# Optimization experiments

Measured on AMD Instinct MI355X. Metric: run time of the kernel, lower is better.

The kernel has to match this reference:

```python
import jax, jax.numpy as jnp
import numpy as np

B, T, E, H = 4, 1024, 1024, 16
D = E // H  # head_size = 64
EPS = 1e-5


def layernorm(x, g, b):
    mu = jnp.mean(x, axis=-1, keepdims=True)
    var = jnp.mean(jnp.square(x - mu), axis=-1, keepdims=True)
    return (x - mu) * jax.lax.rsqrt(var + EPS) * g + b


def setup_inputs() -> dict:
    key = jax.random.key(0)
    ks = jax.random.split(key, 12)
    s = 0.02
    return {
        "x": jax.random.normal(ks[0], (B, T, E), dtype=jnp.float32),
        "ln1_g": jnp.ones((E,), jnp.float32),
        "ln1_b": jnp.zeros((E,), jnp.float32),
        "Wq": jax.random.normal(ks[1], (H, E, D), dtype=jnp.float32) * s,
        "Wk": jax.random.normal(ks[2], (H, E, D), dtype=jnp.float32) * s,
        "Wv": jax.random.normal(ks[3], (H, E, D), dtype=jnp.float32) * s,
        "Wp": jax.random.normal(ks[4], (E, E), dtype=jnp.float32) * s,
        "bp": jnp.zeros((E,), jnp.float32),
        "ln2_g": jnp.ones((E,), jnp.float32),
        "ln2_b": jnp.zeros((E,), jnp.float32),
        "W1": jax.random.normal(ks[5], (E, 4 * E), dtype=jnp.float32) * s,
        "b1": jnp.zeros((4 * E,), jnp.float32),
        "W2": jax.random.normal(ks[6], (4 * E, E), dtype=jnp.float32) * s,
        "b2": jnp.zeros((E,), jnp.float32),
    }


def reference(x, ln1_g, ln1_b, Wq, Wk, Wv, Wp, bp, ln2_g, ln2_b, W1, b1, W2, b2):
    # --- attention sub-block (pre-LN) ---
    h = layernorm(x, ln1_g, ln1_b)               # [B,T,E]
    q = jnp.einsum('bte,hed->bhtd', h, Wq)       # [B,H,T,D]
    k = jnp.einsum('bte,hed->bhtd', h, Wk)
    v = jnp.einsum('bte,hed->bhtd', h, Wv)
    # NOTE: original module has NO 1/sqrt(D) scaling and its 'tril' buffer is
    # all-ones, so masked_fill is a no-op -> full (non-causal) softmax.
    scores = jnp.einsum('bhtd,bhsd->bhts', q, k)  # [B,H,T,T]
    attn = jax.nn.softmax(scores, axis=-1)
    o = jnp.einsum('bhts,bhsd->bhtd', attn, v)    # [B,H,T,D]
    o = o.transpose(0, 2, 1, 3).reshape(x.shape[0], x.shape[1], -1)  # [B,T,E]
    x = x + o @ Wp + bp
    # --- feedforward sub-block (dropout is identity at eval) ---
    h2 = layernorm(x, ln2_g, ln2_b)
    x = x + jax.nn.relu(h2 @ W1 + b1) @ W2 + b2
    return x
```

## Files before the change

### kernel.cpp

```cpp
#include <hip/hip_runtime.h>
#include <hip/hip_bf16.h>

#define BB 4
#define TT 1024
#define EE 1024
#define HH 16
#define DD 64
#define MM 4096
#define NQKV 3072
#define E4 4096

using short8  = __attribute__((ext_vector_type(8))) short;
using short4v = __attribute__((ext_vector_type(4))) short;
using f32x4   = __attribute__((ext_vector_type(4))) float;

__device__ __forceinline__ short f2bf(float f) {
    __hip_bfloat16 h = __float2bfloat16(f);
    return *reinterpret_cast<short*>(&h);
}

__device__ __forceinline__ unsigned int cvtpk_bf16(float a, float b) {
    unsigned int w;
    asm("v_cvt_pk_bf16_f32 %0, %1, %2" : "=v"(w) : "v"(a), "v"(b));
    return w;
}

__device__ __forceinline__ void gld16(const void* g, void* l) {
    __builtin_amdgcn_global_load_lds((__attribute__((address_space(1))) void*)g,
                                     (__attribute__((address_space(3))) void*)l,
                                     16, 0, 0);
}

__global__ __launch_bounds__(256) void tcvt_kernel(const float* __restrict__ in,
                                                   short* __restrict__ out,
                                                   int R, int C) {
    __shared__ short tile[64][65];
    const int c0 = blockIdx.x * 64, r0 = blockIdx.y * 64;
    const int tr = threadIdx.x >> 6;
    const int tc = threadIdx.x & 63;
#pragma unroll
    for (int i = 0; i < 16; ++i) {
        int r = i * 4 + tr;
        tile[tc][r] = f2bf(in[(size_t)(r0 + r) * C + c0 + tc]);
    }
    __syncthreads();
#pragma unroll
    for (int i = 0; i < 16; ++i) {
        int c = i * 4 + tr;
        out[(size_t)(c0 + c) * R + r0 + tc] = tile[c][tc];
    }
}

__global__ __launch_bounds__(256) void pack_qkv_t(const float* __restrict__ Wq,
                                                  const float* __restrict__ Wk,
                                                  const float* __restrict__ Wv,
                                                  short* __restrict__ out) {
    __shared__ short tile[64][65];
    const int m = blockIdx.y;
    const int which = m >> 4, head = m & 15;
    const float* src = ((which == 0) ? Wq : (which == 1) ? Wk : Wv) + (size_t)head * EE * DD;
    const float scale = (which == 1) ? 1.44269504f : 1.0f;
    const int e0 = blockIdx.x * 64;
    const int tr = threadIdx.x >> 6, tc = threadIdx.x & 63;
#pragma unroll
    for (int i = 0; i < 16; ++i) {
        int e = i * 4 + tr;
        tile[tc][e] = f2bf(src[(size_t)(e0 + e) * DD + tc] * scale);
    }
    __syncthreads();
#pragma unroll
    for (int i = 0; i < 16; ++i) {
        int d = i * 4 + tr;
        out[(size_t)(which * 1024 + head * 64 + d) * EE + e0 + tc] = tile[d][tc];
    }
}

__global__ __launch_bounds__(256) void vtr_kernel(const short* __restrict__ qkv,
                                                  short* __restrict__ vT) {
    __shared__ short tile[64][68];
    const int b = blockIdx.z;
    const int t0 = blockIdx.x * 64, c0 = blockIdx.y * 64;
    const int tr = threadIdx.x >> 4;
    const int q4 = (threadIdx.x & 15) * 4;
#pragma unroll
    for (int i = 0; i < 4; ++i) {
        int t = i * 16 + tr;
        short4v v = *(const short4v*)&qkv[((size_t)b * TT + t0 + t) * NQKV + 2048 + c0 + q4];
        *(short4v*)&tile[t][q4] = v;
    }
    __syncthreads();
#pragma unroll
    for (int i = 0; i < 4; ++i) {
        int c = i * 16 + tr;
        short4v v;
        v[0] = tile[q4 + 0][c];
        v[1] = tile[q4 + 1][c];
        v[2] = tile[q4 + 2][c];
        v[3] = tile[q4 + 3][c];
        *(short4v*)&vT[((size_t)b * 1024 + c0 + c) * TT + t0 + q4] = v;
    }
}

__global__ __launch_bounds__(256) void ln_kernel(const float* __restrict__ x,
                                                 const float* __restrict__ g,
                                                 const float* __restrict__ b,
                                                 short* __restrict__ out) {
    __shared__ float red[4];
    const int row = blockIdx.x;
    const int tid = threadIdx.x;
    float4 v = *(const float4*)&x[(size_t)row * EE + tid * 4];
    float s = v.x + v.y + v.z + v.w;
#pragma unroll
    for (int off = 32; off >= 1; off >>= 1) s += __shfl_xor(s, off, 64);
    if ((tid & 63) == 0) red[tid >> 6] = s;
    __syncthreads();
    float mean = (red[0] + red[1] + red[2] + red[3]) * (1.0f / EE);
    __syncthreads();
    float d0 = v.x - mean, d1 = v.y - mean, d2 = v.z - mean, d3 = v.w - mean;
    s = d0 * d0 + d1 * d1 + d2 * d2 + d3 * d3;
#pragma unroll
    for (int off = 32; off >= 1; off >>= 1) s += __shfl_xor(s, off, 64);
    if ((tid & 63) == 0) red[tid >> 6] = s;
    __syncthreads();
    float var = (red[0] + red[1] + red[2] + red[3]) * (1.0f / EE);
    float rstd = rsqrtf(var + 1e-5f);
    int c = tid * 4;
    short4v o;
    o[0] = f2bf(d0 * rstd * g[c + 0] + b[c + 0]);
    o[1] = f2bf(d1 * rstd * g[c + 1] + b[c + 1]);
    o[2] = f2bf(d2 * rstd * g[c + 2] + b[c + 2]);
    o[3] = f2bf(d3 * rstd * g[c + 3] + b[c + 3]);
    *(short4v*)&out[(size_t)row * EE + c] = o;
}

__global__ __launch_bounds__(256) void redk4_kernel(const float* __restrict__ p012,
                                                    const float* __restrict__ p3,
                                                    const float* __restrict__ bias,
                                                    const float* __restrict__ resid,
                                                    float* __restrict__ out) {
    const size_t i = ((size_t)blockIdx.x * 256 + threadIdx.x) * 4;
    float4 a = *(const float4*)&p012[i];
    float4 b = *(const float4*)&p012[i + (size_t)MM * EE];
    float4 c = *(const float4*)&p012[i + (size_t)2 * MM * EE];
    float4 d = *(const float4*)&p3[i];
    float4 r = *(const float4*)&resid[i];
    float4 bb = *(const float4*)&bias[i & 1023];
    float4 o;
    o.x = (a.x + b.x) + (c.x + d.x) + r.x + bb.x;
    o.y = (a.y + b.y) + (c.y + d.y) + r.y + bb.y;
    o.z = (a.z + b.z) + (c.z + d.z) + r.z + bb.z;
    o.w = (a.w + b.w) + (c.w + d.w) + r.w + bb.w;
    *(float4*)&out[i] = o;
}

template <bool HAS_BIAS, bool RELU, bool SPLIT>
__global__ __launch_bounds__(512, 2) void gemm256(const short* __restrict__ A,
                                                  const short* __restrict__ Bt,
                                                  const float* __restrict__ bias,
                                                  void* __restrict__ outp,
                                                  void* __restrict__ outp3,
                                                  int M, int N, int K, int lda) {
    __shared__ __align__(16) short Ab[2][2][8192];
    __shared__ __align__(16) short Bb[2][2][8192];

    const int tid = threadIdx.x;
    const int lane = tid & 63;
    const int wid = tid >> 6;
    const int wr = wid >> 2;
    const int wc = wid & 3;
    const int l15 = lane & 15, lhi = lane >> 4;
    const int rsw = l15 & 7;

    int wg = blockIdx.y * gridDim.x + blockIdx.x;
    const int chunk = (gridDim.x * gridDim.y) >> 3;
    wg = (wg & 7) * chunk + (wg >> 3);
    const int bx = wg % gridDim.x, by = wg / gridDim.x;
    const int row0 = by * 256, col0 = bx * 256;

    const int kb = SPLIT ? blockIdx.z * K : 0;

    const int srow = tid >> 3;
    const int scol = (((tid & 7) ^ (srow & 7)) << 3);

    const int NT = K >> 6;

    f32x4 acc[8][4] = {};

    auto stageA = [&](int b, int h, int k0) {
#pragma unroll
        for (int j = 0; j < 2; ++j)
            gld16(&A[(size_t)(row0 + h * 128 + j * 64 + srow) * lda + kb + k0 + scol],
                  &Ab[b][h][j * 4096 + wid * 512]);
    };
    auto stageB = [&](int b, int h, int k0) {
#pragma unroll
        for (int j = 0; j < 2; ++j)
            gld16(&Bt[(size_t)(col0 + h * 128 + j * 64 + srow) * lda + kb + k0 + scol],
                  &Bb[b][h][j * 4096 + wid * 512]);
    };

    stageA(0, 0, 0); stageA(0, 1, 0);
    stageB(0, 0, 0); stageB(0, 1, 0);
    if (NT > 1) {
        stageB(1, 0, 64); stageB(1, 1, 64);
        asm volatile("s_waitcnt vmcnt(4)" ::: "memory");
    } else {
        asm volatile("s_waitcnt vmcnt(0)" ::: "memory");
    }
    __builtin_amdgcn_s_barrier();

    for (int u = 0; u < NT; ++u) {
        const int buf = u & 1;
        short8 bfr[4][2];
#pragma unroll
        for (int p = 0; p < 4; ++p) {
            if (p == 0) {
#pragma unroll
                for (int n = 0; n < 4; ++n)
#pragma unroll
                    for (int ks = 0; ks < 2; ++ks)
                        bfr[n][ks] = *(const short8*)&Bb[buf][wc >> 1]
                            [((wc & 1) * 64 + n * 16 + l15) * 64 +
                             (((ks << 2) + lhi) ^ rsw) * 8];
            }
            short8 af[2][2];
#pragma unroll
            for (int mi = 0; mi < 2; ++mi)
#pragma unroll
                for (int ks = 0; ks < 2; ++ks)
                    af[mi][ks] = *(const short8*)&Ab[buf][wr]
                        [((p * 2 + mi) * 16 + l15) * 64 +
                         (((ks << 2) + lhi) ^ rsw) * 8];
            if (p == 0 && u + 1 < NT) stageA(buf ^ 1, 0, (u + 1) << 6);
            if (p == 1 && u + 1 < NT) stageA(buf ^ 1, 1, (u + 1) << 6);
            if (p == 2 && u + 2 < NT) stageB(buf, 0, (u + 2) << 6);
            if (p == 3 && u + 2 < NT) stageB(buf, 1, (u + 2) << 6);
            __builtin_amdgcn_s_barrier();
            __builtin_amdgcn_s_setprio(1);
#pragma unroll
            for (int mi = 0; mi < 2; ++mi)
#pragma unroll
                for (int n = 0; n < 4; ++n)
#pragma unroll
                    for (int ks = 0; ks < 2; ++ks)
                        acc[p * 2 + mi][n] = __builtin_amdgcn_mfma_f32_16x16x32_bf16(
                            af[mi][ks], bfr[n][ks], acc[p * 2 + mi][n], 0, 0, 0);
            __builtin_amdgcn_s_setprio(0);
            if (p == 3 && u + 1 < NT) {
                if (u + 2 < NT) asm volatile("s_waitcnt vmcnt(4)" ::: "memory");
                else            asm volatile("s_waitcnt vmcnt(0)" ::: "memory");
            }
            __builtin_amdgcn_s_barrier();
        }
    }

    short* outb = (short*)outp;
    float* outf = nullptr;
    if (SPLIT)
        outf = (blockIdx.z == 3) ? (float*)outp3
                                 : (float*)outp + (size_t)blockIdx.z * M * N;
#pragma unroll
    for (int m = 0; m < 8; ++m)
#pragma unroll
        for (int n = 0; n < 4; ++n)
#pragma unroll
            for (int r = 0; r < 4; ++r) {
                int row = row0 + wr * 128 + m * 16 + lhi * 4 + r;
                int col = col0 + wc * 64 + n * 16 + l15;
                float v = acc[m][n][r];
                if (SPLIT) {
                    outf[(size_t)row * N + col] = v;
                } else {
                    if (HAS_BIAS) v += bias[col];
                    if (RELU) v = fmaxf(v, 0.f);
                    outb[(size_t)row * N + col] = f2bf(v);
                }
            }
}

template <int BN, int PIPE, bool HAS_BIAS, bool RELU, bool RESID, bool OUT_BF16>
__global__ __launch_bounds__(256) void gemm_bt(const short* __restrict__ A,
                                               const short* __restrict__ Bt,
                                               const float* __restrict__ bias,
                                               const float* __restrict__ resid,
                                               void* __restrict__ outp,
                                               int M, int N, int K) {
    constexpr int WRC = (BN == 128) ? 2 : 4;
    constexpr int WCC = (BN == 128) ? 2 : 1;
    constexpr int MI = 8 / WRC;
    constexpr int NI = BN / (16 * WCC);
    constexpr int BCH = BN / 32;
    constexpr int ASZ = 128 * 64, BSZ = BN * 64;

    __shared__ __align__(16) short As[(PIPE ? 2 : 1) * ASZ];
    __shared__ __align__(16) short Bs[(PIPE ? 2 : 1) * BSZ];

    const int tid = threadIdx.x;
    const int lane = tid & 63;
    const int wid = tid >> 6;
    const int wr = (WRC == 2) ? (wid >> 1) : wid;
    const int wc = (WCC == 2) ? (wid & 1) : 0;
    const int l15 = lane & 15, lhi = lane >> 4;

    int wg = blockIdx.y * gridDim.x + blockIdx.x;
    const int chunk = (gridDim.x * gridDim.y) >> 3;
    wg = (wg & 7) * chunk + (wg >> 3);
    const int bx = wg % gridDim.x;
    const int by = wg / gridDim.x;
    const int row0 = by * 128, col0 = bx * BN;

    const int srow = tid >> 3;
    const int scol = (((tid & 7) ^ (srow & 7)) << 3);
    const int rsw = l15 & 7;

    const int wrow0 = wr * (16 * MI);
    const int wcol0 = wc * (16 * NI);

    f32x4 acc[MI][NI] = {};

    auto stage = [&](int k0, int bs) {
#pragma unroll
        for (int ch = 0; ch < 4; ++ch)
            gld16(&A[(size_t)(row0 + ch * 32 + srow) * K + k0 + scol],
                  &As[bs * ASZ + ch * 2048 + wid * 512]);
#pragma unroll
        for (int ch = 0; ch < BCH; ++ch)
            gld16(&Bt[(size_t)(col0 + ch * 32 + srow) * K + k0 + scol],
                  &Bs[bs * BSZ + ch * 2048 + wid * 512]);
    };
    auto compute = [&](int bs) {
#pragma unroll
        for (int ks = 0; ks < 2; ++ks) {
            short8 af[MI], bf[NI];
#pragma unroll
            for (int mi = 0; mi < MI; ++mi)
                af[mi] = *(const short8*)&As[bs * ASZ + (wrow0 + mi * 16 + l15) * 64 +
                                             (((ks << 2) + lhi) ^ rsw) * 8];
#pragma unroll
            for (int ni = 0; ni < NI; ++ni)
                bf[ni] = *(const short8*)&Bs[bs * BSZ + (wcol0 + ni * 16 + l15) * 64 +
                                             (((ks << 2) + lhi) ^ rsw) * 8];
#pragma unroll
            for (int mi = 0; mi < MI; ++mi)
#pragma unroll
                for (int ni = 0; ni < NI; ++ni)
                    acc[mi][ni] = __builtin_amdgcn_mfma_f32_16x16x32_bf16(
                        af[mi], bf[ni], acc[mi][ni], 0, 0, 0);
        }
    };

    if (PIPE == 1) {
        const int nt = K >> 6;
        stage(0, 0);
        stage(64, 1);
        int cur = 0;
        for (int t = 0; t < nt; ++t) {
            if (t + 1 < nt) asm volatile("s_waitcnt vmcnt(6)" ::: "memory");
            else            asm volatile("s_waitcnt vmcnt(0)" ::: "memory");
            __builtin_amdgcn_s_barrier();
            __builtin_amdgcn_sched_barrier(0);
            compute(cur);
            __builtin_amdgcn_sched_barrier(0);
            __builtin_amdgcn_s_barrier();
            if (t + 2 < nt) stage((t + 2) << 6, cur);
            cur ^= 1;
        }
    } else {
        for (int k0 = 0; k0 < K; k0 += 64) {
            __syncthreads();
            stage(k0, 0);
            __syncthreads();
            compute(0);
        }
    }

    float* outf = (float*)outp;
    short* outb = (short*)outp;
#pragma unroll
    for (int mi = 0; mi < MI; ++mi)
#pragma unroll
        for (int ni = 0; ni < NI; ++ni)
#pragma unroll
            for (int r = 0; r < 4; ++r) {
                int row = row0 + wrow0 + mi * 16 + lhi * 4 + r;
                int col = col0 + wcol0 + ni * 16 + l15;
                float v = acc[mi][ni][r];
                if (HAS_BIAS) v += bias[col];
                if (RELU) v = fmaxf(v, 0.f);
                if (RESID) v += resid[(size_t)row * N + col];
                if (OUT_BF16) outb[(size_t)row * N + col] = f2bf(v);
                else outf[(size_t)row * N + col] = v;
            }
}

__global__ __launch_bounds__(256) void attn_kernel(const short* __restrict__ qkv,
                                                   const short* __restrict__ vT,
                                                   short* __restrict__ obuf) {
    __shared__ __align__(16) short Ks[2][64 * 64];
    __shared__ __align__(16) short Vs[2][64 * 64];
    __shared__ __align__(16) unsigned int Pl[4][2][16][40];
    const int tid = threadIdx.x;
    const int lane = tid & 63;
    const int wid = tid >> 6;
    const int l15 = lane & 15, lhi = lane >> 4;
    const int lhi4 = lhi * 4;

    const int nb = ((blockIdx.x & 7) << 6) + (blockIdx.x >> 3);
    const int b = nb >> 7;
    const int h = (nb >> 3) & 15;
    const int q0 = (nb & 7) << 7;
    const size_t rbase = (size_t)b * TT;
    const int hq = h * 64;
    const short* vg = vT + ((size_t)b * 1024 + hq) * TT;

    const int srow = tid >> 3;
    const int scol = (((tid & 7) ^ (srow & 7)) << 3);
    const int rsw = (l15 & 7);

    short8 aq[2][2];
#pragma unroll
    for (int g = 0; g < 2; ++g)
#pragma unroll
        for (int ks = 0; ks < 2; ++ks)
            aq[g][ks] = *(const short8*)&qkv[(rbase + q0 + wid * 32 + g * 16 + l15) * NQKV +
                                             hq + ks * 32 + lhi * 8];

    float mrun[2] = {-INFINITY, -INFINITY};
    float lsum[2] = {0.f, 0.f};
    f32x4 o[2][4] = {};

#pragma unroll
    for (int ch = 0; ch < 2; ++ch) {
        gld16(&qkv[(rbase + 0 + ch * 32 + srow) * NQKV + 1024 + hq + scol],
              &Ks[0][ch * 2048 + wid * 512]);
        gld16(&vg[(size_t)(ch * 32 + srow) * TT + 0 + scol],
              &Vs[0][ch * 2048 + wid * 512]);
    }
    __syncthreads();

    int cur = 0;
    for (int st = 0; st < TT; st += 64) {
        if (st + 64 < TT) {
#pragma unroll
            for (int ch = 0; ch < 2; ++ch) {
                gld16(&qkv[(rbase + st + 64 + ch * 32 + srow) * NQKV + 1024 + hq + scol],
                      &Ks[cur ^ 1][ch * 2048 + wid * 512]);
                gld16(&vg[(size_t)(ch * 32 + srow) * TT + st + 64 + scol],
                      &Vs[cur ^ 1][ch * 2048 + wid * 512]);
            }
        }
        const short* K = &Ks[cur][0];
        const short* V = &Vs[cur][0];

        short8 kf[4][2];
#pragma unroll
        for (int nt = 0; nt < 4; ++nt)
#pragma unroll
            for (int ks = 0; ks < 2; ++ks)
                kf[nt][ks] = *(const short8*)&K[(nt * 16 + l15) * 64 +
                                               (((ks << 2) + lhi) ^ rsw) * 8];

        short8 pa[2][2];
#pragma unroll
        for (int g = 0; g < 2; ++g) {
            f32x4 stv[4] = {};
            __builtin_amdgcn_s_setprio(1);
#pragma unroll
            for (int nt = 0; nt < 4; ++nt)
#pragma unroll
                for (int ks = 0; ks < 2; ++ks)
                    stv[nt] = __builtin_amdgcn_mfma_f32_16x16x32_bf16(
                        kf[nt][ks], aq[g][ks], stv[nt], 0, 0, 0);
            __builtin_amdgcn_s_setprio(0);
            float tn[4];
#pragma unroll
            for (int nt = 0; nt < 4; ++nt)
                tn[nt] = fmaxf(fmaxf(stv[nt][0], stv[nt][1]),
                               fmaxf(stv[nt][2], stv[nt][3]));
            float tm = fmaxf(fmaxf(tn[0], tn[1]), fmaxf(tn[2], tn[3]));
            tm = fmaxf(tm, __shfl_xor(tm, 16, 64));
            tm = fmaxf(tm, __shfl_xor(tm, 32, 64));
            const bool full = !__all(tm - mrun[g] <= 11.5f);
            if (full) {
                float mnew = fmaxf(mrun[g], tm);
                float fac = exp2f(mrun[g] - mnew);
                mrun[g] = mnew;
                lsum[g] *= fac;
                float f0 = __shfl(fac, lhi4 + 0, 64);
                float f1 = __shfl(fac, lhi4 + 1, 64);
                float f2 = __shfl(fac, lhi4 + 2, 64);
                float f3 = __shfl(fac, lhi4 + 3, 64);
#pragma unroll
                for (int dt = 0; dt < 4; ++dt) {
                    o[g][dt][0] *= f0; o[g][dt][1] *= f1;
                    o[g][dt][2] *= f2; o[g][dt][3] *= f3;
                }
            }
            float pv[4][4];
            float sn[4];
#pragma unroll
            for (int nt = 0; nt < 4; ++nt) {
#pragma unroll
                for (int r = 0; r < 4; ++r) pv[nt][r] = exp2f(stv[nt][r] - mrun[g]);
                sn[nt] = (pv[nt][0] + pv[nt][1]) + (pv[nt][2] + pv[nt][3]);
            }
            float rs = (sn[0] + sn[1]) + (sn[2] + sn[3]);
            rs += __shfl_xor(rs, 16, 64);
            rs += __shfl_xor(rs, 32, 64);
            lsum[g] += rs;
#pragma unroll
            for (int nt = 0; nt < 4; ++nt) {
                uint2 ww;
                ww.x = cvtpk_bf16(pv[nt][0], pv[nt][1]);
                ww.y = cvtpk_bf16(pv[nt][2], pv[nt][3]);
                *(uint2*)&Pl[wid][g][l15][nt * 8 + lhi * 2] = ww;
            }
            pa[g][0] = *(const short8*)&Pl[wid][g][l15][lhi4];
            pa[g][1] = *(const short8*)&Pl[wid][g][l15][16 + lhi4];
        }

        short8 vf[4][2];
#pragma unroll
        for (int dt = 0; dt < 4; ++dt)
#pragma unroll
            for (int k2 = 0; k2 < 2; ++k2)
                vf[dt][k2] = *(const short8*)&V[(dt * 16 + l15) * 64 +
                                               (((k2 << 2) + lhi) ^ rsw) * 8];
        __builtin_amdgcn_s_setprio(1);
#pragma unroll
        for (int g = 0; g < 2; ++g)
#pragma unroll
            for (int dt = 0; dt < 4; ++dt)
#pragma unroll
                for (int k2 = 0; k2 < 2; ++k2)
                    o[g][dt] = __builtin_amdgcn_mfma_f32_16x16x32_bf16(
                        pa[g][k2], vf[dt][k2], o[g][dt], 0, 0, 0);
        __builtin_amdgcn_s_setprio(0);

        __syncthreads();
        cur ^= 1;
    }
#pragma unroll
    for (int g = 0; g < 2; ++g) {
        float inv = 1.0f / lsum[g];
        float i0 = __shfl(inv, lhi4 + 0, 64);
        float i1 = __shfl(inv, lhi4 + 1, 64);
        float i2 = __shfl(inv, lhi4 + 2, 64);
        float i3 = __shfl(inv, lhi4 + 3, 64);
#pragma unroll
        for (int dt = 0; dt < 4; ++dt) {
            int col = hq + dt * 16 + l15;
            size_t rw = rbase + q0 + wid * 32 + g * 16 + lhi4;
            obuf[(rw + 0) * EE + col] = f2bf(o[g][dt][0] * i0);
            obuf[(rw + 1) * EE + col] = f2bf(o[g][dt][1] * i1);
            obuf[(rw + 2) * EE + col] = f2bf(o[g][dt][2] * i2);
            obuf[(rw + 3) * EE + col] = f2bf(o[g][dt][3] * i3);
        }
    }
}

extern "C" void kernel_launch(void* const* d_in, const int* in_sizes, int n_in,
                              void* d_out, int out_size, void* d_ws, size_t ws_size,
                              hipStream_t stream) {
    const float* x   = (const float*)d_in[0];
    const float* g1  = (const float*)d_in[1];
    const float* be1 = (const float*)d_in[2];
    const float* Wq  = (const float*)d_in[3];
    const float* Wk  = (const float*)d_in[4];
    const float* Wv  = (const float*)d_in[5];
    const float* Wp  = (const float*)d_in[6];
    const float* bp  = (const float*)d_in[7];
    const float* g2  = (const float*)d_in[8];
    const float* be2 = (const float*)d_in[9];
    const float* W1  = (const float*)d_in[10];
    const float* b1f = (const float*)d_in[11];
    const float* W2  = (const float*)d_in[12];
    const float* b2f = (const float*)d_in[13];

    char* p = (char*)d_ws;
    short* h_bf   = (short*)p; p += (size_t)MM * EE * 2;
    short* wqkv   = (short*)p; p += (size_t)EE * NQKV * 2;
    short* qkv    = (short*)p; p += (size_t)MM * NQKV * 2;
    short* o_bf   = (short*)p; p += (size_t)MM * EE * 2;
    short* wp_bf  = (short*)p; p += (size_t)EE * EE * 2;
    float* x1     = (float*)p; p += (size_t)MM * EE * 4;
    short* h2_bf  = (short*)p; p += (size_t)MM * EE * 2;
    short* w1_bf  = (short*)p; p += (size_t)EE * E4 * 2;
    short* mid_bf = (short*)p; p += (size_t)MM * E4 * 2;
    short* w2_bf  = (short*)p; p += (size_t)E4 * EE * 2;
    short* vTb    = (short*)p; p += (size_t)BB * 1024 * TT * 2;

    float* part012 = (float*)d_ws;
    float* part3   = (float*)h2_bf;

    pack_qkv_t<<<dim3(16, 48), 256, 0, stream>>>(Wq, Wk, Wv, wqkv);
    tcvt_kernel<<<dim3(16, 16), 256, 0, stream>>>(Wp, wp_bf, EE, EE);
    tcvt_kernel<<<dim3(64, 16), 256, 0, stream>>>(W1, w1_bf, EE, E4);
    tcvt_kernel<<<dim3(16, 64), 256, 0, stream>>>(W2, w2_bf, E4, EE);

    ln_kernel<<<MM, 256, 0, stream>>>(x, g1, be1, h_bf);

    gemm256<false, false, false>
        <<<dim3(NQKV / 256, MM / 256), 512, 0, stream>>>(h_bf, wqkv, nullptr,
                                                         qkv, nullptr, MM, NQKV, EE, EE);

    vtr_kernel<<<dim3(16, 16, BB), 256, 0, stream>>>(qkv, vTb);

    attn_kernel<<<BB * HH * (TT / 128), 256, 0, stream>>>(qkv, vTb, o_bf);

    gemm_bt<64, 1, true, false, true, false>
        <<<dim3(EE / 64, MM / 128), 256, 0, stream>>>(o_bf, wp_bf, bp, x, x1, MM, EE, EE);

    ln_kernel<<<MM, 256, 0, stream>>>(x1, g2, be2, h2_bf);

    gemm256<true, true, false>
        <<<dim3(E4 / 256, MM / 256), 512, 0, stream>>>(h2_bf, w1_bf, b1f,
                                                       mid_bf, nullptr, MM, E4, EE, EE);

    gemm256<false, false, true>
        <<<dim3(EE / 256, MM / 256, 4), 512, 0, stream>>>(mid_bf, w2_bf, nullptr,
                                                          part012, part3,
                                                          MM, EE, 1024, E4);
    redk4_kernel<<<(MM * EE / 4) / 256, 256, 0, stream>>>(part012, part3, b2f, x1,
                                                          (float*)d_out);
}
```

Baseline: 225.5 us.

## Enlarge attention blocks to 256 queries and 128-key tiles with 8 waves

The attention kernel now runs 512 threads per block covering 256 query rows, and stages 128 keys per iteration instead of 64. Each staged K/V tile is reused by twice as many waves, and the kernel does half as many barrier and double-buffer iterations. The V tile uses a new 128-wide swizzled layout, and the P scratch buffer shrinks to one slot per wave. The cost is more LDS per block and half as many blocks (256), which may reduce occupancy and load balance across CUs.

```diff
diff --git a/kernel.cpp b/kernel.cpp
--- a/kernel.cpp
+++ b/kernel.cpp
@@ -393,29 +393,31 @@
             }
 }
 
-__global__ __launch_bounds__(256) void attn_kernel(const short* __restrict__ qkv,
+__global__ __launch_bounds__(512) void attn_kernel(const short* __restrict__ qkv,
                                                    const short* __restrict__ vT,
                                                    short* __restrict__ obuf) {
-    __shared__ __align__(16) short Ks[2][64 * 64];
-    __shared__ __align__(16) short Vs[2][64 * 64];
-    __shared__ __align__(16) unsigned int Pl[4][2][16][40];
+    __shared__ __align__(16) short Ks[2][128 * 64];
+    __shared__ __align__(16) short Vs[2][64 * 128];
+    __shared__ __align__(16) unsigned int Pl[8][16][40];
     const int tid = threadIdx.x;
     const int lane = tid & 63;
     const int wid = tid >> 6;
     const int l15 = lane & 15, lhi = lane >> 4;
     const int lhi4 = lhi * 4;
 
-    const int nb = ((blockIdx.x & 7) << 6) + (blockIdx.x >> 3);
-    const int b = nb >> 7;
-    const int h = (nb >> 3) & 15;
-    const int q0 = (nb & 7) << 7;
+    const int nb = ((blockIdx.x & 7) << 5) + (blockIdx.x >> 3);
+    const int b = nb >> 6;
+    const int h = (nb >> 2) & 15;
+    const int q0 = (nb & 3) << 8;
     const size_t rbase = (size_t)b * TT;
     const int hq = h * 64;
     const short* vg = vT + ((size_t)b * 1024 + hq) * TT;
 
     const int srow = tid >> 3;
     const int scol = (((tid & 7) ^ (srow & 7)) << 3);
-    const int rsw = (l15 & 7);
+    const int vrow = tid >> 4;
+    const int vscol = ((tid & 15) ^ (vrow & 7)) << 3;
+    const int rsw = l15 & 7;
 
     short8 aq[2][2];
 #pragma unroll
@@ -429,113 +431,112 @@
     float lsum[2] = {0.f, 0.f};
     f32x4 o[2][4] = {};
 
-#pragma unroll
-    for (int ch = 0; ch < 2; ++ch) {
-        gld16(&qkv[(rbase + 0 + ch * 32 + srow) * NQKV + 1024 + hq + scol],
-              &Ks[0][ch * 2048 + wid * 512]);
-        gld16(&vg[(size_t)(ch * 32 + srow) * TT + 0 + scol],
-              &Vs[0][ch * 2048 + wid * 512]);
-    }
+    auto stage = [&](int buf, int st) {
+#pragma unroll
+        for (int ch = 0; ch < 2; ++ch)
+            gld16(&qkv[(rbase + st + ch * 64 + srow) * NQKV + 1024 + hq + scol],
+                  &Ks[buf][ch * 4096 + wid * 512]);
+#pragma unroll
+        for (int ch = 0; ch < 2; ++ch)
+            gld16(&vg[(size_t)(ch * 32 + vrow) * TT + st + vscol],
+                  &Vs[buf][ch * 4096 + wid * 512]);
+    };
+
+    stage(0, 0);
     __syncthreads();
 
     int cur = 0;
-    for (int st = 0; st < TT; st += 64) {
-        if (st + 64 < TT) {
-#pragma unroll
-            for (int ch = 0; ch < 2; ++ch) {
-                gld16(&qkv[(rbase + st + 64 + ch * 32 + srow) * NQKV + 1024 + hq + scol],
-                      &Ks[cur ^ 1][ch * 2048 + wid * 512]);
-                gld16(&vg[(size_t)(ch * 32 + srow) * TT + st + 64 + scol],
-                      &Vs[cur ^ 1][ch * 2048 + wid * 512]);
-            }
-        }
+    for (int st = 0; st < TT; st += 128) {
+        if (st + 128 < TT) stage(cur ^ 1, st + 128);
         const short* K = &Ks[cur][0];
         const short* V = &Vs[cur][0];
 
-        short8 kf[4][2];
-#pragma unroll
-        for (int nt = 0; nt < 4; ++nt)
-#pragma unroll
-            for (int ks = 0; ks < 2; ++ks)
-                kf[nt][ks] = *(const short8*)&K[(nt * 16 + l15) * 64 +
-                                               (((ks << 2) + lhi) ^ rsw) * 8];
-
-        short8 pa[2][2];
-#pragma unroll
-        for (int g = 0; g < 2; ++g) {
-            f32x4 stv[4] = {};
+#pragma unroll
+        for (int h2 = 0; h2 < 2; ++h2) {
+            short8 kf[4][2];
+#pragma unroll
+            for (int nt = 0; nt < 4; ++nt)
+#pragma unroll
+                for (int ks = 0; ks < 2; ++ks)
+                    kf[nt][ks] = *(const short8*)&K[(h2 * 64 + nt * 16 + l15) * 64 +
+                                                   (((ks << 2) + lhi) ^ rsw) * 8];
+
+            short8 pa[2][2];
+#pragma unroll
+            for (int g = 0; g < 2; ++g) {
+                f32x4 stv[4] = {};
+                __builtin_amdgcn_s_setprio(1);
+#pragma unroll
+                for (int nt = 0; nt < 4; ++nt)
+#pragma unroll
+                    for (int ks = 0; ks < 2; ++ks)
+                        stv[nt] = __builtin_amdgcn_mfma_f32_16x16x32_bf16(
+                            kf[nt][ks], aq[g][ks], stv[nt], 0, 0, 0);
+                __builtin_amdgcn_s_setprio(0);
+                float tn[4];
+#pragma unroll
+                for (int nt = 0; nt < 4; ++nt)
+                    tn[nt] = fmaxf(fmaxf(stv[nt][0], stv[nt][1]),
+                                   fmaxf(stv[nt][2], stv[nt][3]));
+                float tm = fmaxf(fmaxf(tn[0], tn[1]), fmaxf(tn[2], tn[3]));
+                tm = fmaxf(tm, __shfl_xor(tm, 16, 64));
+                tm = fmaxf(tm, __shfl_xor(tm, 32, 64));
+                const bool full = !__all(tm - mrun[g] <= 11.5f);
+                if (full) {
+                    float mnew = fmaxf(mrun[g], tm);
+                    float fac = exp2f(mrun[g] - mnew);
+                    mrun[g] = mnew;
+                    lsum[g] *= fac;
+                    float f0 = __shfl(fac, lhi4 + 0, 64);
+                    float f1 = __shfl(fac, lhi4 + 1, 64);
+                    float f2 = __shfl(fac, lhi4 + 2, 64);
+                    float f3 = __shfl(fac, lhi4 + 3, 64);
+#pragma unroll
+                    for (int dt = 0; dt < 4; ++dt) {
+                        o[g][dt][0] *= f0; o[g][dt][1] *= f1;
+                        o[g][dt][2] *= f2; o[g][dt][3] *= f3;
+                    }
+                }
+                float pv[4][4], sn[4];
+#pragma unroll
+                for (int nt = 0; nt < 4; ++nt) {
+#pragma unroll
+                    for (int r = 0; r < 4; ++r) pv[nt][r] = exp2f(stv[nt][r] - mrun[g]);
+                    sn[nt] = (pv[nt][0] + pv[nt][1]) + (pv[nt][2] + pv[nt][3]);
+                }
+                float rs = (sn[0] + sn[1]) + (sn[2] + sn[3]);
+                rs += __shfl_xor(rs, 16, 64);
+                rs += __shfl_xor(rs, 32, 64);
+                lsum[g] += rs;
+#pragma unroll
+                for (int nt = 0; nt < 4; ++nt) {
+                    uint2 ww;
+                    ww.x = cvtpk_bf16(pv[nt][0], pv[nt][1]);
+                    ww.y = cvtpk_bf16(pv[nt][2], pv[nt][3]);
+                    *(uint2*)&Pl[wid][l15][nt * 8 + lhi * 2] = ww;
+                }
+                pa[g][0] = *(const short8*)&Pl[wid][l15][lhi4];
+                pa[g][1] = *(const short8*)&Pl[wid][l15][16 + lhi4];
+            }
+
+            short8 vf[4][2];
+#pragma unroll
+            for (int dt = 0; dt < 4; ++dt)
+#pragma unroll
+                for (int k2 = 0; k2 < 2; ++k2)
+                    vf[dt][k2] = *(const short8*)&V[(dt * 16 + l15) * 128 +
+                                                   ((h2 << 3) + (((k2 << 2) + lhi) ^ rsw)) * 8];
             __builtin_amdgcn_s_setprio(1);
 #pragma unroll
-            for (int nt = 0; nt < 4; ++nt)
-#pragma unroll
-                for (int ks = 0; ks < 2; ++ks)
-                    stv[nt] = __builtin_amdgcn_mfma_f32_16x16x32_bf16(
-                        kf[nt][ks], aq[g][ks], stv[nt], 0, 0, 0);
+            for (int g = 0; g < 2; ++g)
+#pragma unroll
+                for (int dt = 0; dt < 4; ++dt)
+#pragma unroll
+                    for (int k2 = 0; k2 < 2; ++k2)
+                        o[g][dt] = __builtin_amdgcn_mfma_f32_16x16x32_bf16(
+                            pa[g][k2], vf[dt][k2], o[g][dt], 0, 0, 0);
             __builtin_amdgcn_s_setprio(0);
-            float tn[4];
-#pragma unroll
-            for (int nt = 0; nt < 4; ++nt)
-                tn[nt] = fmaxf(fmaxf(stv[nt][0], stv[nt][1]),
-                               fmaxf(stv[nt][2], stv[nt][3]));
-            float tm = fmaxf(fmaxf(tn[0], tn[1]), fmaxf(tn[2], tn[3]));
-            tm = fmaxf(tm, __shfl_xor(tm, 16, 64));
-            tm = fmaxf(tm, __shfl_xor(tm, 32, 64));
-            const bool full = !__all(tm - mrun[g] <= 11.5f);
-            if (full) {
-                float mnew = fmaxf(mrun[g], tm);
-                float fac = exp2f(mrun[g] - mnew);
-                mrun[g] = mnew;
-                lsum[g] *= fac;
-                float f0 = __shfl(fac, lhi4 + 0, 64);
-                float f1 = __shfl(fac, lhi4 + 1, 64);
-                float f2 = __shfl(fac, lhi4 + 2, 64);
-                float f3 = __shfl(fac, lhi4 + 3, 64);
-#pragma unroll
-                for (int dt = 0; dt < 4; ++dt) {
-                    o[g][dt][0] *= f0; o[g][dt][1] *= f1;
-                    o[g][dt][2] *= f2; o[g][dt][3] *= f3;
-                }
-            }
-            float pv[4][4];
-            float sn[4];
-#pragma unroll
-            for (int nt = 0; nt < 4; ++nt) {
-#pragma unroll
-                for (int r = 0; r < 4; ++r) pv[nt][r] = exp2f(stv[nt][r] - mrun[g]);
-                sn[nt] = (pv[nt][0] + pv[nt][1]) + (pv[nt][2] + pv[nt][3]);
-            }
-            float rs = (sn[0] + sn[1]) + (sn[2] + sn[3]);
-            rs += __shfl_xor(rs, 16, 64);
-            rs += __shfl_xor(rs, 32, 64);
-            lsum[g] += rs;
-#pragma unroll
-            for (int nt = 0; nt < 4; ++nt) {
-                uint2 ww;
-                ww.x = cvtpk_bf16(pv[nt][0], pv[nt][1]);
-                ww.y = cvtpk_bf16(pv[nt][2], pv[nt][3]);
-                *(uint2*)&Pl[wid][g][l15][nt * 8 + lhi * 2] = ww;
-            }
-            pa[g][0] = *(const short8*)&Pl[wid][g][l15][lhi4];
-            pa[g][1] = *(const short8*)&Pl[wid][g][l15][16 + lhi4];
         }
-
-        short8 vf[4][2];
-#pragma unroll
-        for (int dt = 0; dt < 4; ++dt)
-#pragma unroll
-            for (int k2 = 0; k2 < 2; ++k2)
-                vf[dt][k2] = *(const short8*)&V[(dt * 16 + l15) * 64 +
-                                               (((k2 << 2) + lhi) ^ rsw) * 8];
-        __builtin_amdgcn_s_setprio(1);
-#pragma unroll
-        for (int g = 0; g < 2; ++g)
-#pragma unroll
-            for (int dt = 0; dt < 4; ++dt)
-#pragma unroll
-                for (int k2 = 0; k2 < 2; ++k2)
-                    o[g][dt] = __builtin_amdgcn_mfma_f32_16x16x32_bf16(
-                        pa[g][k2], vf[dt][k2], o[g][dt], 0, 0, 0);
-        __builtin_amdgcn_s_setprio(0);
 
         __syncthreads();
         cur ^= 1;
@@ -606,7 +607,7 @@
 
     vtr_kernel<<<dim3(16, 16, BB), 256, 0, stream>>>(qkv, vTb);
 
-    attn_kernel<<<BB * HH * (TT / 128), 256, 0, stream>>>(qkv, vTb, o_bf);
+    attn_kernel<<<BB * HH * (TT / 256), 512, 0, stream>>>(qkv, vTb, o_bf);
 
     gemm_bt<64, 1, true, false, true, false>
         <<<dim3(EE / 64, MM / 128), 256, 0, stream>>>(o_bf, wp_bf, bp, x, x1, MM, EE, EE);
```

Result: no change. 221.9 us (-1.6%).

## Split attention over two KV halves with separate combine kernel

Applied to the files above, without the earlier changes.

Doubles the attention grid by giving each block half of the key/value sequence, writing unnormalized fp32 partial outputs plus running max and sum. A new combine kernel merges the two halves with log-sum-exp weights and writes the bf16 head-interleaved output. This aims to raise occupancy and parallelism on a grid that was small relative to the CU count, at the cost of extra fp32 partial traffic and an additional launch. Partials reuse existing workspace buffers.

```diff
diff --git a/kernel.cpp b/kernel.cpp
--- a/kernel.cpp
+++ b/kernel.cpp
@@ -151,6 +151,27 @@
     o.z = (a.z + b.z) + (c.z + d.z) + r.z + bb.z;
     o.w = (a.w + b.w) + (c.w + d.w) + r.w + bb.w;
     *(float4*)&out[i] = o;
+}
+
+__global__ __launch_bounds__(256) void comb_kernel(const float* __restrict__ pO,
+                                                   const float2* __restrict__ pml,
+                                                   short* __restrict__ obuf) {
+    const int row = blockIdx.x * 16 + (threadIdx.x >> 4);
+    const int d = (threadIdx.x & 15) * 4;
+    float2 ml0 = pml[row];
+    float2 ml1 = pml[row + 65536];
+    float m = fmaxf(ml0.x, ml1.x);
+    float w0 = exp2f(ml0.x - m), w1 = exp2f(ml1.x - m);
+    float inv = 1.0f / (w0 * ml0.y + w1 * ml1.y);
+    float4 O0 = *(const float4*)&pO[(size_t)row * 64 + d];
+    float4 O1 = *(const float4*)&pO[(size_t)(row + 65536) * 64 + d];
+    short4v s;
+    s[0] = f2bf((O0.x * w0 + O1.x * w1) * inv);
+    s[1] = f2bf((O0.y * w0 + O1.y * w1) * inv);
+    s[2] = f2bf((O0.z * w0 + O1.z * w1) * inv);
+    s[3] = f2bf((O0.w * w0 + O1.w * w1) * inv);
+    const int b = row >> 14, h = (row >> 10) & 15, q = row & 1023;
+    *(short4v*)&obuf[((size_t)b * 1024 + q) * EE + h * 64 + d] = s;
 }
 
 template <bool HAS_BIAS, bool RELU, bool SPLIT>
@@ -395,20 +416,23 @@
 
 __global__ __launch_bounds__(256) void attn_kernel(const short* __restrict__ qkv,
                                                    const short* __restrict__ vT,
-                                                   short* __restrict__ obuf) {
+                                                   float* __restrict__ pO,
+                                                   float2* __restrict__ pml) {
     __shared__ __align__(16) short Ks[2][64 * 64];
     __shared__ __align__(16) short Vs[2][64 * 64];
-    __shared__ __align__(16) unsigned int Pl[4][2][16][40];
+    __shared__ __align__(16) unsigned int Pl[4][16][44];
     const int tid = threadIdx.x;
     const int lane = tid & 63;
     const int wid = tid >> 6;
     const int l15 = lane & 15, lhi = lane >> 4;
     const int lhi4 = lhi * 4;
 
-    const int nb = ((blockIdx.x & 7) << 6) + (blockIdx.x >> 3);
-    const int b = nb >> 7;
-    const int h = (nb >> 3) & 15;
-    const int q0 = (nb & 7) << 7;
+    const int nb = ((blockIdx.x & 7) << 7) + (blockIdx.x >> 3);
+    const int b = nb >> 8;
+    const int h = (nb >> 4) & 15;
+    const int q0 = ((nb >> 1) & 7) << 7;
+    const int z = nb & 1;
+    const int kv0 = z << 9;
     const size_t rbase = (size_t)b * TT;
     const int hq = h * 64;
     const short* vg = vT + ((size_t)b * 1024 + hq) * TT;
@@ -431,16 +455,16 @@
 
 #pragma unroll
     for (int ch = 0; ch < 2; ++ch) {
-        gld16(&qkv[(rbase + 0 + ch * 32 + srow) * NQKV + 1024 + hq + scol],
+        gld16(&qkv[(rbase + kv0 + ch * 32 + srow) * NQKV + 1024 + hq + scol],
               &Ks[0][ch * 2048 + wid * 512]);
-        gld16(&vg[(size_t)(ch * 32 + srow) * TT + 0 + scol],
+        gld16(&vg[(size_t)(ch * 32 + srow) * TT + kv0 + scol],
               &Vs[0][ch * 2048 + wid * 512]);
     }
     __syncthreads();
 
     int cur = 0;
-    for (int st = 0; st < TT; st += 64) {
-        if (st + 64 < TT) {
+    for (int st = kv0; st < kv0 + 512; st += 64) {
+        if (st + 64 < kv0 + 512) {
 #pragma unroll
             for (int ch = 0; ch < 2; ++ch) {
                 gld16(&qkv[(rbase + st + 64 + ch * 32 + srow) * NQKV + 1024 + hq + scol],
@@ -513,10 +537,10 @@
                 uint2 ww;
                 ww.x = cvtpk_bf16(pv[nt][0], pv[nt][1]);
                 ww.y = cvtpk_bf16(pv[nt][2], pv[nt][3]);
-                *(uint2*)&Pl[wid][g][l15][nt * 8 + lhi * 2] = ww;
-            }
-            pa[g][0] = *(const short8*)&Pl[wid][g][l15][lhi4];
-            pa[g][1] = *(const short8*)&Pl[wid][g][l15][16 + lhi4];
+                *(uint2*)&Pl[wid][l15][nt * 8 + lhi * 2] = ww;
+            }
+            pa[g][0] = *(const short8*)&Pl[wid][l15][lhi4];
+            pa[g][1] = *(const short8*)&Pl[wid][l15][16 + lhi4];
         }
 
         short8 vf[4][2];
@@ -540,22 +564,20 @@
         __syncthreads();
         cur ^= 1;
     }
+
+    const size_t prow0 = (size_t)(z * 64 + b * 16 + h) * 1024;
 #pragma unroll
     for (int g = 0; g < 2; ++g) {
-        float inv = 1.0f / lsum[g];
-        float i0 = __shfl(inv, lhi4 + 0, 64);
-        float i1 = __shfl(inv, lhi4 + 1, 64);
-        float i2 = __shfl(inv, lhi4 + 2, 64);
-        float i3 = __shfl(inv, lhi4 + 3, 64);
-#pragma unroll
-        for (int dt = 0; dt < 4; ++dt) {
-            int col = hq + dt * 16 + l15;
-            size_t rw = rbase + q0 + wid * 32 + g * 16 + lhi4;
-            obuf[(rw + 0) * EE + col] = f2bf(o[g][dt][0] * i0);
-            obuf[(rw + 1) * EE + col] = f2bf(o[g][dt][1] * i1);
-            obuf[(rw + 2) * EE + col] = f2bf(o[g][dt][2] * i2);
-            obuf[(rw + 3) * EE + col] = f2bf(o[g][dt][3] * i3);
+        if (lhi == 0) {
+            float2 t; t.x = mrun[g]; t.y = lsum[g];
+            pml[prow0 + q0 + wid * 32 + g * 16 + l15] = t;
         }
+#pragma unroll
+        for (int dt = 0; dt < 4; ++dt)
+#pragma unroll
+            for (int r = 0; r < 4; ++r)
+                pO[(prow0 + q0 + wid * 32 + g * 16 + lhi4 + r) * 64 + dt * 16 + l15] =
+                    o[g][dt][r];
     }
 }
 
@@ -590,6 +612,9 @@
     short* w2_bf  = (short*)p; p += (size_t)E4 * EE * 2;
     short* vTb    = (short*)p; p += (size_t)BB * 1024 * TT * 2;
 
+    float*  attn_pO  = (float*)mid_bf;
+    float2* attn_pml = (float2*)h_bf;
+
     float* part012 = (float*)d_ws;
     float* part3   = (float*)h2_bf;
 
@@ -606,7 +631,9 @@
 
     vtr_kernel<<<dim3(16, 16, BB), 256, 0, stream>>>(qkv, vTb);
 
-    attn_kernel<<<BB * HH * (TT / 128), 256, 0, stream>>>(qkv, vTb, o_bf);
+    attn_kernel<<<BB * HH * (TT / 128) * 2, 256, 0, stream>>>(qkv, vTb,
+                                                              attn_pO, attn_pml);
+    comb_kernel<<<(BB * HH * TT) / 16, 256, 0, stream>>>(attn_pO, attn_pml, o_bf);
 
     gemm_bt<64, 1, true, false, true, false>
         <<<dim3(EE / 64, MM / 128), 256, 0, stream>>>(o_bf, wp_bf, bp, x, x1, MM, EE, EE);
```

Result: slower. 235.6 us (+4.5%).
